# Performance work log

Measured on AMD Instinct MI355X. Metric: run time of the kernel, lower is better.

Reference implementation:

```python
import jax, jax.numpy as jnp
import numpy as np

E, B, S, D, F = 8, 2, 1024, 1024, 4096


def setup_inputs() -> dict:
    key = jax.random.key(0)
    ks = jax.random.split(key, 9)
    sc_d = 1.0 / np.sqrt(D)
    sc_f = 1.0 / np.sqrt(F)
    hidden_states = jax.random.normal(ks[0], (B, S, D), dtype=jnp.float32)
    # router outputs set externally on the parent model in the original code
    gating_probs = jax.nn.softmax(jax.random.normal(ks[1], (B, E), dtype=jnp.float32), axis=-1)
    shared_gate_prob = jax.nn.sigmoid(jax.random.normal(ks[2], (B, 1), dtype=jnp.float32))
    # stacked expert SwiGLU MLP weights (Llama-style gate/up/down)
    Wg = jax.random.normal(ks[3], (E, D, F), dtype=jnp.float32) * sc_d
    Wu = jax.random.normal(ks[4], (E, D, F), dtype=jnp.float32) * sc_d
    Wd = jax.random.normal(ks[5], (E, F, D), dtype=jnp.float32) * sc_f
    # shared expert MLP
    Sg = jax.random.normal(ks[6], (D, F), dtype=jnp.float32) * sc_d
    Su = jax.random.normal(ks[7], (D, F), dtype=jnp.float32) * sc_d
    Sd = jax.random.normal(ks[8], (F, D), dtype=jnp.float32) * sc_f
    return {
        "hidden_states": hidden_states,
        "gating_probs": gating_probs,
        "shared_gate_prob": shared_gate_prob,
        "Wg": Wg, "Wu": Wu, "Wd": Wd,
        "Sg": Sg, "Su": Su, "Sd": Sd,
    }


def reference(hidden_states, gating_probs, shared_gate_prob, Wg, Wu, Wd, Sg, Su, Sd):
    h = hidden_states  # [B,S,D]
    # every expert's MLP runs on all tokens (naive all-experts-dense, as in source)
    g = jnp.einsum("bsd,edf->ebsf", h, Wg)
    u = jnp.einsum("bsd,edf->ebsf", h, Wu)
    expert_outs = jnp.einsum("ebsf,efd->ebsd", jax.nn.silu(g) * u, Wd)  # [E,B,S,D]
    # weighted_sum routing with per-sequence gating probs [B,E]
    expert_output = jnp.einsum("be,ebsd->bsd", gating_probs, expert_outs)
    # shared expert MLP
    shared = jnp.einsum("bsf,fd->bsd", jax.nn.silu(h @ Sg) * (h @ Su), Sd)
    sg = shared_gate_prob[:, :, None]  # [B,1,1]
    return (1.0 - sg) * expert_output + sg * shared
```

## Files before the change

kernel.cpp:

```cpp
#include <hip/hip_runtime.h>
#include <cstdio>
#include <cstdint>

typedef _Float16 f16;
typedef _Float16 f16x4 __attribute__((ext_vector_type(4)));
typedef _Float16 f16x8 __attribute__((ext_vector_type(8)));
typedef float f32x4 __attribute__((ext_vector_type(4)));

#define GLL16(gp, lp)                                                          \
  __builtin_amdgcn_global_load_lds(                                            \
      (const __attribute__((address_space(1))) void*)(gp),                     \
      (__attribute__((address_space(3))) void*)(lp), 16, 0, 0)

#define BARX __builtin_amdgcn_s_barrier()
#define WAITV4 { asm volatile("s_waitcnt vmcnt(4)" ::: "memory"); __builtin_amdgcn_sched_barrier(0); }
#define WAITV0 { asm volatile("s_waitcnt vmcnt(0)" ::: "memory"); __builtin_amdgcn_sched_barrier(0); }
#define WAITL0 { asm volatile("s_waitcnt lgkmcnt(0)" ::: "memory"); __builtin_amdgcn_sched_barrier(0); }

__global__ void cvt_f32_f16_kernel(const float* __restrict__ in,
                                   f16* __restrict__ out, int n4) {
  int i = blockIdx.x * blockDim.x + threadIdx.x;
  if (i < n4) {
    f32x4 v = reinterpret_cast<const f32x4*>(in)[i];
    f16x4 o;
    o[0] = (f16)v[0]; o[1] = (f16)v[1]; o[2] = (f16)v[2]; o[3] = (f16)v[3];
    reinterpret_cast<f16x4*>(out)[i] = o;
  }
}

__global__ void tr_cvt2_kernel(const float* __restrict__ inA,
                               const float* __restrict__ inB,
                               f16* __restrict__ out, size_t slotOff,
                               int C, size_t OS, int nA) {
  int slot = blockIdx.z;
  const float* src = (slot < nA) ? inA + (size_t)slot * 64 * gridDim.y * C : inB;
  f16* dst = out + (size_t)slot * slotOff;
  __shared__ f16 tl[4096];
  int t = threadIdx.x;
  int r0 = blockIdx.y * 64, c0 = blockIdx.x * 64;
  int br = (t >> 4) * 4, bc = (t & 15) * 4;
  f32x4 v[4];
#pragma unroll
  for (int i = 0; i < 4; ++i)
    v[i] = *(const f32x4*)&src[(size_t)(r0 + br + i) * C + c0 + bc];
#pragma unroll
  for (int cc = 0; cc < 4; ++cc) {
    int c = bc + cc;
    f16x4 o;
    o[0] = (f16)v[0][cc]; o[1] = (f16)v[1][cc];
    o[2] = (f16)v[2][cc]; o[3] = (f16)v[3][cc];
    *(f16x4*)&tl[c * 64 + (br ^ ((c & 7) * 8))] = o;
  }
  __syncthreads();
  int rw = (t & 7) * 8, cw = t >> 3;
#pragma unroll
  for (int j = 0; j < 2; ++j) {
    int c = cw + j * 32;
    f16x8 o = *(const f16x8*)&tl[c * 64 + (rw ^ ((c & 7) * 8))];
    *(f16x8*)&dst[(size_t)(c0 + c) * OS + r0 + rw] = o;
  }
}

#define STAGE_A3(NB)                                                           \
  do {                                                                         \
    f16* d_ = &lds[(NB) * 16384 + ldsT];                                       \
    GLL16(aS, d_); GLL16(aS + 65536, d_ + 4096);                               \
    GLL16(aS + 131072, d_ + 8192); GLL16(aS + 196608, d_ + 12288);             \
  } while (0)
#define STAGE_G3(NB)                                                           \
  do {                                                                         \
    f16* d_ = &lds[32768 + (NB) * 16384 + ldsT];                               \
    GLL16(gS, d_); GLL16(gS + 65536, d_ + 4096);                               \
  } while (0)
#define STAGE_U3(NB)                                                           \
  do {                                                                         \
    f16* d_ = &lds[32768 + (NB) * 16384 + 8192 + ldsT];                        \
    GLL16(uS, d_); GLL16(uS + 65536, d_ + 4096);                               \
  } while (0)

#define RD3(BUF, VK)                                                           \
  do {                                                                         \
    const f16* pa_ = &lds[(BUF) * 16384 + wr * 4096 + vRow + (VK)];            \
    aF[0] = *(const f16x8*)(pa_);                                              \
    aF[1] = *(const f16x8*)(pa_ + 1024);                                       \
    aF[2] = *(const f16x8*)(pa_ + 2048);                                       \
    aF[3] = *(const f16x8*)(pa_ + 3072);                                       \
    const f16* pg_ = &lds[32768 + (BUF) * 16384 + wc * 4096 + vRow + (VK)];    \
    bG[0] = *(const f16x8*)(pg_);                                              \
    bG[1] = *(const f16x8*)(pg_ + 1024);                                       \
    bG[2] = *(const f16x8*)(pg_ + 2048);                                       \
    bG[3] = *(const f16x8*)(pg_ + 3072);                                       \
    const f16* pu_ = pg_ + 8192;                                               \
    bU[0] = *(const f16x8*)(pu_);                                              \
    bU[1] = *(const f16x8*)(pu_ + 1024);                                       \
    bU[2] = *(const f16x8*)(pu_ + 2048);                                       \
    bU[3] = *(const f16x8*)(pu_ + 3072);                                       \
  } while (0)

#define MFMA32()                                                               \
  do {                                                                         \
    __builtin_amdgcn_s_setprio(1);                                             \
    _Pragma("unroll") for (int mi = 0; mi < 4; ++mi)                           \
        _Pragma("unroll") for (int ni = 0; ni < 4; ++ni) {                     \
      ag[mi][ni] = __builtin_amdgcn_mfma_f32_16x16x32_f16(aF[mi], bG[ni],      \
                                                          ag[mi][ni], 0, 0, 0);\
      au[mi][ni] = __builtin_amdgcn_mfma_f32_16x16x32_f16(aF[mi], bU[ni],      \
                                                          au[mi][ni], 0, 0, 0);\
    }                                                                          \
    __builtin_amdgcn_s_setprio(0);                                             \
    __builtin_amdgcn_sched_barrier(0);                                         \
  } while (0)

#define BODY3(BUF, DOSTA, DOSTB)                                               \
  do {                                                                         \
    RD3(BUF, vK0);                                                             \
    if (DOSTA) { STAGE_A3((BUF) ^ 1); }                                        \
    BARX; WAITL0;                                                              \
    MFMA32();                                                                  \
    BARX;                                                                      \
    RD3(BUF, vK1);                                                             \
    if (DOSTB) {                                                               \
      STAGE_G3((BUF) ^ 1); STAGE_U3((BUF) ^ 1);                                \
      aS += 64; gS += 64; uS += 64;                                            \
    }                                                                          \
    BARX; WAITL0;                                                              \
    MFMA32();                                                                  \
    if (DOSTB) { WAITV0; }                                                     \
    BARX;                                                                      \
  } while (0)

__global__ __launch_bounds__(512, 2) void gemmUG3_kernel(
    const f16* __restrict__ A, const f16* __restrict__ Bg,
    const f16* __restrict__ Bu, f16* __restrict__ T,
    const float* __restrict__ gate, const float* __restrict__ sgp) {
  __shared__ __align__(16) f16 lds[65536];

  int lgl = (blockIdx.x & 7) * 288 + (blockIdx.x >> 3);
  int mt = lgl & 7;
  int ntg = lgl >> 3;
  int slot = ntg >> 5;

  int t = threadIdx.x, w = t >> 6, l = t & 63;
  int wr = w >> 1, wc = w & 1;

  int kqs = (((t & 7) ^ ((t >> 3) & 7)) * 8);
  const f16* aS = A + (size_t)(mt * 256 + (t >> 3)) * 1024 + kqs;
  const f16* gS = Bg + (size_t)slot * 4194304 +
                  (size_t)((ntg & 31) * 128 + (t >> 3)) * 1024 + kqs;
  const f16* uS = Bu + (size_t)slot * 4194304 +
                  (size_t)((ntg & 31) * 128 + (t >> 3)) * 1024 + kqs;
  int ldsT = t * 8;

  int vRow = (l & 15) * 64;
  int vK0 = (((l >> 4) ^ (l & 7))) * 8;
  int vK1 = (((4 + (l >> 4)) ^ (l & 7))) * 8;

  f16x8 aF[4], bG[4], bU[4];
  f32x4 ag[4][4] = {}, au[4][4] = {};

  STAGE_A3(0); STAGE_G3(0); STAGE_U3(0);
  aS += 64; gS += 64; uS += 64;
  WAITV0; BARX;

#pragma unroll 1
  for (int it = 0; it < 7; ++it) {
    BODY3(0, 1, 1);
    BODY3(1, 1, 1);
  }
  BODY3(0, 1, 1);
  BODY3(1, 0, 0);

  int r0 = (l >> 4) * 4, c0 = l & 15;
  int rowb = mt * 256 + wr * 64;
  size_t colb = (size_t)ntg * 128 + wc * 64;
  int b = mt >> 2;
  float s = sgp[b];
  float coef = (slot < 8) ? (1.f - s) * gate[b * 8 + slot] : s;
#pragma unroll
  for (int mi = 0; mi < 4; ++mi) {
#pragma unroll
    for (int ni = 0; ni < 4; ++ni) {
#pragma unroll
      for (int j = 0; j < 4; ++j) {
        float g = ag[mi][ni][j];
        float u = au[mi][ni][j];
        T[(size_t)(rowb + mi * 16 + r0 + j) * 36864 + colb + ni * 16 + c0] =
            (f16)(g / (1.f + __expf(-g)) * u * coef);
      }
    }
  }
}

#define STAGE_A(tile, hf)                                                      \
  do {                                                                         \
    const f16* g_ = Abase + (size_t)((hf) * 128) * LD + (tile) * 64 + aVoff;   \
    f16* d_ = &lds[(2 * ((tile) & 1) + (hf)) * 8192 + w * 512];                \
    GLL16(g_, d_);                                                             \
    GLL16(g_ + (size_t)64 * LD, d_ + 4096);                                    \
  } while (0)
#define STAGE_B(tile, hf)                                                      \
  do {                                                                         \
    const f16* g_ = Bbase + (size_t)((hf) * 128) * LD + (tile) * 64 + aVoff;   \
    f16* d_ = &lds[32768 + (2 * ((tile) & 1) + (hf)) * 8192 + w * 512];        \
    GLL16(g_, d_);                                                             \
    GLL16(g_ + (size_t)64 * LD, d_ + 4096);                                    \
  } while (0)

#define RD_A(rh, buf)                                                          \
  do {                                                                         \
    const f16* p_ = &lds[(2 * (buf) + wr) * 8192 + (rh) * 4096];               \
    aFd[0][0] = *(const f16x8*)(p_ + 0 * 1024 + vR0);                          \
    aFd[0][1] = *(const f16x8*)(p_ + 0 * 1024 + vR1);                          \
    aFd[1][0] = *(const f16x8*)(p_ + 1 * 1024 + vR0);                          \
    aFd[1][1] = *(const f16x8*)(p_ + 1 * 1024 + vR1);                          \
    aFd[2][0] = *(const f16x8*)(p_ + 2 * 1024 + vR0);                          \
    aFd[2][1] = *(const f16x8*)(p_ + 2 * 1024 + vR1);                          \
    aFd[3][0] = *(const f16x8*)(p_ + 3 * 1024 + vR0);                          \
    aFd[3][1] = *(const f16x8*)(p_ + 3 * 1024 + vR1);                          \
  } while (0)
#define RD_B(ch, buf)                                                          \
  do {                                                                         \
    const f16* p_ = &lds[32768 + (2 * (buf) + bh) * 8192 + bq * 4096 +         \
                         (ch) * 2 * 1024];                                     \
    bFd[(ch) * 2][0] = *(const f16x8*)(p_ + vR0);                              \
    bFd[(ch) * 2][1] = *(const f16x8*)(p_ + vR1);                              \
    bFd[(ch) * 2 + 1][0] = *(const f16x8*)(p_ + 1024 + vR0);                   \
    bFd[(ch) * 2 + 1][1] = *(const f16x8*)(p_ + 1024 + vR1);                   \
  } while (0)

#define MFMA16(rh, ch)                                                         \
  do {                                                                         \
    __builtin_amdgcn_s_setprio(1);                                             \
    _Pragma("unroll") for (int rt = 0; rt < 4; ++rt)                           \
        _Pragma("unroll") for (int ct = 0; ct < 2; ++ct)                       \
        _Pragma("unroll") for (int ks = 0; ks < 2; ++ks)                       \
            acc[(rh) * 4 + rt][(ch) * 2 + ct] =                                \
        __builtin_amdgcn_mfma_f32_16x16x32_f16(                                \
            aFd[rt][ks], bFd[(ch) * 2 + ct][ks],                               \
            acc[(rh) * 4 + rt][(ch) * 2 + ct], 0, 0, 0);                       \
    __builtin_amdgcn_s_setprio(0);                                             \
    __builtin_amdgcn_sched_barrier(0);                                         \
  } while (0)

__global__ __launch_bounds__(512, 2) void gemmD_kernel(
    const f16* __restrict__ A, const f16* __restrict__ B,
    float* __restrict__ P) {
  constexpr size_t LD = 36864;
  constexpr int NTILES = 72;
  __shared__ __align__(16) f16 lds[65536];

  int wg = (blockIdx.x & 7) * 32 + (blockIdx.x >> 3);
  int kpart = wg >> 5, mt = (wg >> 2) & 7, nt = wg & 3;

  int t = threadIdx.x, w = t >> 6, l = t & 63;
  int wr = w >> 2, wc = w & 3;
  int bh = wc >> 1, bq = wc & 1;

  int scol = (((l & 7) ^ ((l >> 3) & 7)) * 8);
  size_t stRow = (size_t)(w * 8 + (l >> 3)) * LD;
  size_t aVoff = stRow + scol;
  const f16* Abase = A + (size_t)mt * 256 * LD + (size_t)kpart * 4608;
  const f16* Bbase = B + (size_t)nt * 256 * LD + (size_t)kpart * 4608;

  int vR0 = (l & 15) * 64 + (((l >> 4) * 8) ^ ((l & 7) * 8));
  int vR1 = (l & 15) * 64 + ((32 + (l >> 4) * 8) ^ ((l & 7) * 8));

  f16x8 aFd[4][2], bFd[4][2];
  f32x4 acc[8][4] = {};

  STAGE_B(0, 0); STAGE_B(0, 1);
  STAGE_A(0, 0); STAGE_A(0, 1);
  STAGE_B(1, 0); STAGE_B(1, 1);
  WAITV4;
  BARX;

#pragma unroll 1
  for (int it = 0; it < NTILES / 2 - 1; ++it) {
    int t1 = 2 * it + 1, t2 = 2 * it + 2, t3 = 2 * it + 3;
    RD_A(0, 0); RD_B(0, 0); STAGE_A(t1, 0);
    BARX; WAITL0; MFMA16(0, 0); BARX;
    RD_B(1, 0); STAGE_A(t1, 1);
    BARX; WAITL0; MFMA16(0, 1); BARX;
    RD_A(1, 0); STAGE_B(t2, 0);
    BARX; WAITL0; MFMA16(1, 0); BARX;
    STAGE_B(t2, 1);
    BARX; MFMA16(1, 1); WAITV4; BARX;
    RD_A(0, 1); RD_B(0, 1); STAGE_A(t2, 0);
    BARX; WAITL0; MFMA16(0, 0); BARX;
    RD_B(1, 1); STAGE_A(t2, 1);
    BARX; WAITL0; MFMA16(0, 1); BARX;
    RD_A(1, 1); STAGE_B(t3, 0);
    BARX; WAITL0; MFMA16(1, 0); BARX;
    STAGE_B(t3, 1);
    BARX; MFMA16(1, 1); WAITV4; BARX;
  }
  RD_A(0, 0); RD_B(0, 0); STAGE_A(NTILES - 1, 0);
  BARX; WAITL0; MFMA16(0, 0); BARX;
  RD_B(1, 0); STAGE_A(NTILES - 1, 1);
  BARX; WAITL0; MFMA16(0, 1); BARX;
  RD_A(1, 0);
  BARX; WAITL0; MFMA16(1, 0); BARX;
  BARX; MFMA16(1, 1); WAITV0; BARX;
  RD_A(0, 1); RD_B(0, 1);
  BARX; WAITL0; MFMA16(0, 0); BARX;
  RD_B(1, 1);
  BARX; WAITL0; MFMA16(0, 1); BARX;
  RD_A(1, 1);
  BARX; WAITL0; MFMA16(1, 0); BARX;
  MFMA16(1, 1);

  int r0 = (l >> 4) * 4, c0 = l & 15;
  size_t base = ((size_t)kpart << 21);
  int rowbase = mt * 256 + wr * 128;
  int colbase = nt * 256 + wc * 64;
#pragma unroll
  for (int rt = 0; rt < 8; ++rt)
#pragma unroll
    for (int ct = 0; ct < 4; ++ct)
#pragma unroll
      for (int j = 0; j < 4; ++j)
        P[base + (size_t)(rowbase + rt * 16 + r0 + j) * 1024 + colbase +
          ct * 16 + c0] = acc[rt][ct][j];
}

__global__ void reduce8_kernel(const float* __restrict__ P,
                               float* __restrict__ out, int n4) {
  int i = blockIdx.x * blockDim.x + threadIdx.x;
  if (i < n4) {
    f32x4 s = {0.f, 0.f, 0.f, 0.f};
#pragma unroll
    for (int e = 0; e < 8; ++e) {
      f32x4 v = reinterpret_cast<const f32x4*>(P + ((size_t)e << 21))[i];
      s += v;
    }
    reinterpret_cast<f32x4*>(out)[i] = s;
  }
}

extern "C" void kernel_launch(void* const* d_in, const int* in_sizes, int n_in,
                              void* d_out, int out_size, void* d_ws,
                              size_t ws_size, hipStream_t stream) {
  const float* h    = (const float*)d_in[0];
  const float* gate = (const float*)d_in[1];
  const float* sgp  = (const float*)d_in[2];
  const float* Wg   = (const float*)d_in[3];
  const float* Wu   = (const float*)d_in[4];
  const float* Wd   = (const float*)d_in[5];
  const float* Sg   = (const float*)d_in[6];
  const float* Su   = (const float*)d_in[7];
  const float* Sd   = (const float*)d_in[8];

  const size_t SZ_HB = 4194304;
  const size_t SZ_W  = 75497472;
  const size_t SZ_T  = 150994944;
  const size_t SZ_P  = 67108864;
  char* ws = (char*)d_ws;
  f16*   hb  = (f16*)(ws);
  f16*   WgT = (f16*)(ws + SZ_HB);
  f16*   WuT = (f16*)(ws + SZ_HB + SZ_W);
  f16*   WdT = (f16*)(ws + SZ_HB + 2 * SZ_W);
  f16*   T   = (f16*)(ws + SZ_HB + 3 * SZ_W);
  float* P   = (float*)(ws + SZ_HB + 3 * SZ_W + SZ_T);
  size_t need = SZ_HB + 3 * SZ_W + SZ_T + SZ_P;
  if (ws_size < need) {
    fprintf(stderr, "kernel_launch: ws too small (%zu < %zu)\n", ws_size, need);
    return;
  }
  float* out = (float*)d_out;

  cvt_f32_f16_kernel<<<2048, 256, 0, stream>>>(h, hb, 524288);
  tr_cvt2_kernel<<<dim3(64, 16, 9), 256, 0, stream>>>(
      Wg, Sg, WgT, 4096ull * 1024, 4096, 1024, 8);
  tr_cvt2_kernel<<<dim3(64, 16, 9), 256, 0, stream>>>(
      Wu, Su, WuT, 4096ull * 1024, 4096, 1024, 8);
  tr_cvt2_kernel<<<dim3(16, 64, 9), 256, 0, stream>>>(
      Wd, Sd, WdT, 4096, 1024, 36864, 8);

  gemmUG3_kernel<<<2304, 512, 0, stream>>>(hb, WgT, WuT, T, gate, sgp);
  gemmD_kernel<<<256, 512, 0, stream>>>(T, WdT, P);
  reduce8_kernel<<<2048, 256, 0, stream>>>(P, out, 524288);
}
```

Measured before the change: 576.6 us.

## Prefetch two K-tiles ahead in fused gate/up GEMM with partial vmcnt waits

Reworks the gate/up GEMM main loop so global-to-LDS loads for a tile are issued two iterations ahead instead of one. Both LDS fragment reads for a buffer finish before a single barrier, and that same buffer is then refilled while the second MFMA batch runs. The wait becomes vmcnt(8) instead of vmcnt(0), so one tile's loads stay in flight across iterations. This is meant to hide global memory latency and cut the barriers per iteration from four to two. The cost is more outstanding loads, and correctness depends on the fragment reads finishing before the buffer is overwritten.

```diff
diff --git a/kernel.cpp b/kernel.cpp
--- a/kernel.cpp
+++ b/kernel.cpp
@@ -13,6 +13,7 @@
       (__attribute__((address_space(3))) void*)(lp), 16, 0, 0)
 
 #define BARX __builtin_amdgcn_s_barrier()
+#define WAITV8 { asm volatile("s_waitcnt vmcnt(8)" ::: "memory"); __builtin_amdgcn_sched_barrier(0); }
 #define WAITV4 { asm volatile("s_waitcnt vmcnt(4)" ::: "memory"); __builtin_amdgcn_sched_barrier(0); }
 #define WAITV0 { asm volatile("s_waitcnt vmcnt(0)" ::: "memory"); __builtin_amdgcn_sched_barrier(0); }
 #define WAITL0 { asm volatile("s_waitcnt lgkmcnt(0)" ::: "memory"); __builtin_amdgcn_sched_barrier(0); }
@@ -61,21 +62,17 @@
   }
 }
 
-#define STAGE_A3(NB)                                                           \
-  do {                                                                         \
-    f16* d_ = &lds[(NB) * 16384 + ldsT];                                       \
-    GLL16(aS, d_); GLL16(aS + 65536, d_ + 4096);                               \
-    GLL16(aS + 131072, d_ + 8192); GLL16(aS + 196608, d_ + 12288);             \
-  } while (0)
-#define STAGE_G3(NB)                                                           \
-  do {                                                                         \
-    f16* d_ = &lds[32768 + (NB) * 16384 + ldsT];                               \
-    GLL16(gS, d_); GLL16(gS + 65536, d_ + 4096);                               \
-  } while (0)
-#define STAGE_U3(NB)                                                           \
-  do {                                                                         \
-    f16* d_ = &lds[32768 + (NB) * 16384 + 8192 + ldsT];                        \
-    GLL16(uS, d_); GLL16(uS + 65536, d_ + 4096);                               \
+#define STAGE_T(NB, TILE)                                                      \
+  do {                                                                         \
+    const f16* a_ = aS + (size_t)(TILE) * 64;                                  \
+    f16* da_ = &lds[(NB) * 16384 + ldsT];                                      \
+    GLL16(a_, da_); GLL16(a_ + 65536, da_ + 4096);                             \
+    GLL16(a_ + 131072, da_ + 8192); GLL16(a_ + 196608, da_ + 12288);           \
+    const f16* g_ = gS + (size_t)(TILE) * 64;                                  \
+    f16* dg_ = &lds[32768 + (NB) * 16384 + ldsT];                              \
+    GLL16(g_, dg_); GLL16(g_ + 65536, dg_ + 4096);                             \
+    const f16* u_ = uS + (size_t)(TILE) * 64;                                  \
+    GLL16(u_, dg_ + 8192); GLL16(u_ + 65536, dg_ + 12288);                     \
   } while (0)
 
 #define RD3(BUF, VK)                                                           \
@@ -111,21 +108,17 @@
     __builtin_amdgcn_sched_barrier(0);                                         \
   } while (0)
 
-#define BODY3(BUF, DOSTA, DOSTB)                                               \
+#define BODY4(BUF, TILE, DOST, WV)                                             \
   do {                                                                         \
     RD3(BUF, vK0);                                                             \
-    if (DOSTA) { STAGE_A3((BUF) ^ 1); }                                        \
-    BARX; WAITL0;                                                              \
+    WAITL0;                                                                    \
     MFMA32();                                                                  \
+    RD3(BUF, vK1);                                                             \
+    WAITL0;                                                                    \
     BARX;                                                                      \
-    RD3(BUF, vK1);                                                             \
-    if (DOSTB) {                                                               \
-      STAGE_G3((BUF) ^ 1); STAGE_U3((BUF) ^ 1);                                \
-      aS += 64; gS += 64; uS += 64;                                            \
-    }                                                                          \
-    BARX; WAITL0;                                                              \
+    if (DOST) { STAGE_T(BUF, TILE); }                                          \
     MFMA32();                                                                  \
-    if (DOSTB) { WAITV0; }                                                     \
+    WV;                                                                        \
     BARX;                                                                      \
   } while (0)
 
@@ -158,17 +151,17 @@
   f16x8 aF[4], bG[4], bU[4];
   f32x4 ag[4][4] = {}, au[4][4] = {};
 
-  STAGE_A3(0); STAGE_G3(0); STAGE_U3(0);
-  aS += 64; gS += 64; uS += 64;
-  WAITV0; BARX;
+  STAGE_T(0, 0);
+  STAGE_T(1, 1);
+  WAITV8; BARX;
 
 #pragma unroll 1
   for (int it = 0; it < 7; ++it) {
-    BODY3(0, 1, 1);
-    BODY3(1, 1, 1);
-  }
-  BODY3(0, 1, 1);
-  BODY3(1, 0, 0);
+    BODY4(0, 2 * it + 2, 1, WAITV8);
+    BODY4(1, 2 * it + 3, 1, WAITV8);
+  }
+  BODY4(0, 0, 0, WAITV0);
+  BODY4(1, 0, 0, {});
 
   int r0 = (l >> 4) * 4, c0 = l & 15;
   int rowb = mt * 256 + wr * 64;
```

New measurement: 564.8 us. -2.0%, faster.
